# Optimization experiments

Measured on AMD Instinct MI355X. Metric: run time of the kernel, lower is better.

## Reference

```python
import jax, jax.numpy as jnp
import numpy as np

N_SEQ = 512      # n: number of generation steps (rows of x_tensor)
N_POOL = 4096    # candidate node pool size (rows of f_tensor / a_tensor)
N_FEAT = 20
E = 64           # n_node_embed
G = 128          # n_graph_embed
S = 16           # n_seq_embed
ALPHA = 20       # n_seq_alphabets


def setup_inputs() -> dict:
    key = jax.random.key(0)
    ks = jax.random.split(key, 16)
    f32 = jnp.float32

    def lin(k, fan_in, shape):
        return jax.random.normal(k, shape, f32) / jnp.sqrt(jnp.asarray(fan_in, f32))

    return {
        "x_tensor": jax.random.normal(ks[0], (N_SEQ, ALPHA), f32),
        "f_tensor": jax.random.normal(ks[1], (N_POOL, N_FEAT), f32),
        "a_tensor": jax.random.uniform(ks[2], (N_POOL, N_POOL), f32),
        "d_tensor": jax.random.uniform(ks[3], (N_POOL, N_POOL), f32),
        "w_feat": lin(ks[4], N_FEAT, (N_FEAT, E)),
        "b_feat": lin(ks[5], N_FEAT, (E,)),
        "w_gcn1": lin(ks[6], E, (E, E)),   # GCN W1, bias=False
        "w_gcn2": lin(ks[7], E, (E, E)),   # GCN W1, bias=False
        "w_graph": lin(ks[8], E, (E, G)),
        "b_graph": lin(ks[9], E, (G,)),
        "w_gate": lin(ks[10], E, (E, G)),
        "b_gate": lin(ks[11], E, (G,)),
        "w_edge": lin(ks[12], 2 * E + S + G, (2 * E + S + G, 1)),
        "b_edge": lin(ks[13], 2 * E + S + G, (1,)),
        "w_seq": lin(ks[14], ALPHA, (ALPHA, S)),
        "b_seq": lin(ks[15], ALPHA, (S,)),
    }


def reference(x_tensor, f_tensor, a_tensor, d_tensor,
              w_feat, b_feat, w_gcn1, w_gcn2,
              w_graph, b_graph, w_gate, b_gate,
              w_edge, b_edge, w_seq, b_seq):
    n = x_tensor.shape[0]
    Np = f_tensor.shape[0]
    e = w_feat.shape[1]
    g_dim = w_graph.shape[1]

    seq_embed = x_tensor @ w_seq + b_seq                 # [n, S]
    f_nodes_in = f_tensor @ w_feat + b_feat              # [Np, E]
    dAd = (d_tensor @ a_tensor) @ d_tensor               # gcn1: D A D
    h_nodes_in = (dAd @ jax.nn.relu(f_nodes_in)) @ w_gcn1  # [Np, E]

    # Chain graph at step k has k+1 nodes; A = I + sub/super diagonals.
    # Degrees: 1 (k==0), 2 at endpoints, 3 interior. Dh[k, i] = deg^{-1/2}, masked.
    ii = jnp.arange(n)
    kk = ii[:, None]
    jj = ii[None, :]
    deg = jnp.where((jj == 0) | (jj == kk), 2.0, 3.0)
    deg = jnp.where(kk == 0, 1.0, deg)
    Dh = jnp.where(jj <= kk, deg ** -0.5, 0.0).astype(x_tensor.dtype)  # [n, n]

    def step(carry, k):
        mask, idxs, h_last, h_graph = carry
        z = jnp.concatenate([
            h_nodes_in,
            jnp.broadcast_to(h_last, (Np, e)),
            jnp.broadcast_to(seq_embed[k], (Np, seq_embed.shape[1])),
            jnp.broadcast_to(h_graph, (Np, g_dim)),
        ], axis=1)                                        # [Np, 2E+S+G]
        score = ((jax.nn.relu(z) * mask[:, None]) @ w_edge)[:, 0] + b_edge[0]
        idx = jnp.argmax(score)
        mask = mask.at[idx].set(0.0)
        idxs = idxs.at[k].set(idx.astype(jnp.int32))

        # gcn2 on the chain graph over the k+1 selected nodes (band-structured).
        F_sel = f_nodes_in[idxs]                          # [n, E]; rows > k masked by dh
        dh = Dh[k]                                        # [n]
        gmat = dh[:, None] * F_sel
        g_up = jnp.pad(gmat, ((0, 1), (0, 0)))[1:]        # g[i+1]
        g_dn = jnp.pad(gmat, ((1, 0), (0, 0)))[:-1]       # g[i-1]
        dF = dh[:, None] * (gmat + g_up + g_dn)           # (D A D) F on the chain
        h_nodes = dF @ w_gcn2                             # [n, E]; rows > k are zero
        h_last_new = jnp.take(h_nodes, k, axis=0)

        valid = (jnp.arange(n) <= k).astype(h_nodes.dtype)[:, None]
        hg = h_nodes @ w_graph + b_graph
        gg = h_nodes @ w_gate + b_gate
        h_graph_new = jnp.sum(hg * jax.nn.sigmoid(gg) * valid, axis=0)
        return (mask, idxs, h_last_new, h_graph_new), score

    init = (jnp.ones(Np, x_tensor.dtype),
            jnp.zeros(n, jnp.int32),
            jnp.zeros(e, x_tensor.dtype),
            jnp.zeros(g_dim, x_tensor.dtype))
    (_, idxs, _, _), scores = jax.lax.scan(step, init, jnp.arange(n))
    return scores, idxs
```

## Files before the change

kernel.cpp:

```cpp
#include <hip/hip_runtime.h>
#include <math.h>

#define NPOOL 4096
#define NSEQ  512
#define NF    20
#define EDIM  64
#define GDIM  128
#define SDIM  16
#define ALPH  20
#define SPLITK 32
#define KSLICE (NPOOL / SPLITK)

__device__ __forceinline__ double relu_d(double x){ return x > 0.0 ? x : 0.0; }
__device__ __forceinline__ double sigm_d(double x){ return 1.0 / (1.0 + exp(-x)); }

__device__ __forceinline__ unsigned long long sortable_u64(double x) {
    x = x + 0.0;
    unsigned long long b = (unsigned long long)__double_as_longlong(x);
    return b ^ ((b >> 63) ? ~0ULL : 0x8000000000000000ULL);
}

__global__ __launch_bounds__(256) void k_prep(const float* __restrict__ f, const float* __restrict__ wf,
                       const float* __restrict__ bf, double* __restrict__ Fin, double* __restrict__ R,
                       double* __restrict__ T1z, double* __restrict__ T2z, double* __restrict__ T3z) {
    int t = blockIdx.x * 256 + threadIdx.x;
    int i = t >> 6, e = t & 63;
    double acc = (double)bf[e];
#pragma unroll
    for (int j = 0; j < NF; ++j)
        acc += (double)f[i * NF + j] * (double)wf[j * EDIM + e];
    Fin[t] = acc;
    R[t] = acc > 0.0 ? acc : 0.0;
    T1z[t] = 0.0; T2z[t] = 0.0; T3z[t] = 0.0;
}

__global__ __launch_bounds__(256) void k_seqe(const float* __restrict__ x, const float* __restrict__ wsq,
                       const float* __restrict__ bsq, double* __restrict__ seqe, int* __restrict__ rank) {
    int t = blockIdx.x * 256 + threadIdx.x;
    int k = t >> 4, s = t & 15;
    double acc = (double)bsq[s];
#pragma unroll
    for (int q = 0; q < ALPH; ++q)
        acc += (double)x[k * ALPH + q] * (double)wsq[q * SDIM + s];
    seqe[t] = acc;
    if (t < NPOOL) rank[t] = 1 << 30;
}

__global__ __launch_bounds__(256, 4) void gemm_f64_v5(const float* __restrict__ A, const double* __restrict__ B,
                                                      double* __restrict__ C) {
    __shared__ double As[32][66];
    __shared__ double Bs[32][66];
    int t  = threadIdx.x;
    int tx = t & 15;
    int ty = t >> 4;
    int row0 = blockIdx.x * 64;
    int k0   = blockIdx.y * KSLICE;
    double acc[4][4] = {};
    for (int kt = k0; kt < k0 + KSLICE; kt += 32) {
        {
            int r = t >> 2, kq = t & 3;
            const float* Ap = A + (size_t)(row0 + r) * NPOOL + kt + kq * 8;
            float4 f0 = *(const float4*)Ap;
            float4 f1 = *(const float4*)(Ap + 4);
            int kb = kq * 8;
            int rs = r ^ (kq << 2);
            As[kb + 0][rs] = (double)f0.x; As[kb + 1][rs] = (double)f0.y;
            As[kb + 2][rs] = (double)f0.z; As[kb + 3][rs] = (double)f0.w;
            As[kb + 4][rs] = (double)f1.x; As[kb + 5][rs] = (double)f1.y;
            As[kb + 6][rs] = (double)f1.z; As[kb + 7][rs] = (double)f1.w;
        }
#pragma unroll
        for (int it = 0; it < 8; ++it) {
            int l = t + 256 * it;
            int kr = l >> 6, cc = l & 63;
            Bs[kr][cc] = B[(size_t)(kt + kr) * 64 + cc];
        }
        __syncthreads();
#pragma unroll
        for (int kk = 0; kk < 32; ++kk) {
            int s = ((kk >> 3) & 3) << 2;
            double2 a01 = *(const double2*)&As[kk][(2 * ty +  0) ^ s];
            double2 a23 = *(const double2*)&As[kk][(2 * ty + 32) ^ s];
            double2 b01 = *(const double2*)&Bs[kk][2 * tx];
            double2 b23 = *(const double2*)&Bs[kk][2 * tx + 32];
            double a[4] = {a01.x, a01.y, a23.x, a23.y};
            double b[4] = {b01.x, b01.y, b23.x, b23.y};
#pragma unroll
            for (int i = 0; i < 4; ++i)
#pragma unroll
                for (int j = 0; j < 4; ++j)
                    acc[i][j] = fma(a[i], b[j], acc[i][j]);
        }
        __syncthreads();
    }
    int rr[4] = {2 * ty, 2 * ty + 1, 2 * ty + 32, 2 * ty + 33};
    int cc[4] = {2 * tx, 2 * tx + 1, 2 * tx + 32, 2 * tx + 33};
#pragma unroll
    for (int i = 0; i < 4; ++i)
#pragma unroll
        for (int j = 0; j < 4; ++j)
            unsafeAtomicAdd(&C[(size_t)(row0 + rr[i]) * 64 + cc[j]], acc[i][j]);
}

__global__ __launch_bounds__(256) void k_head(const double* __restrict__ T3, const float* __restrict__ w1,
                       const float* __restrict__ we, double* __restrict__ s) {
    __shared__ float w1s[64 * 64];
    int tt = threadIdx.x;
    for (int i = tt; i < 64 * 64; i += 256) w1s[i] = w1[i];
    __syncthreads();
    int row = (blockIdx.x * 256 + tt) >> 6;
    int e = tt & 63;
    const double* r = T3 + (size_t)row * 64;
    double h = 0.0;
#pragma unroll
    for (int c = 0; c < 64; ++c)
        h += r[c] * (double)w1s[c * 64 + e];
    double p = (h > 0.0 ? h : 0.0) * (double)we[e];
    for (int off = 32; off; off >>= 1) p += __shfl_down(p, off, 64);
    if (e == 0) s[row] = p;
}

__global__ __launch_bounds__(1024) void k_sort3(const double* __restrict__ s, int* __restrict__ order,
                        double* __restrict__ skey, int* __restrict__ orderB) {
    __shared__ unsigned long long P[NPOOL];
    __shared__ int idxF[NPOOL];
    __shared__ int fbS;
    int t = threadIdx.x;
    if (t == 0) fbS = 0;
    unsigned long long v[4];
#pragma unroll
    for (int i = 0; i < 4; ++i) {
        int e = 4 * t + i;
        unsigned long long srt = sortable_u64(s[e]);
        v[i] = ((~(srt >> 12)) << 12) | (unsigned long long)e;
    }

#define SHFL_ROUND(jj, kk)                                                        \
    {                                                                             \
        int lm = (int)((jj) >> 2);                                                \
        _Pragma("unroll")                                                         \
        for (int i = 0; i < 4; ++i) {                                             \
            unsigned long long p = (unsigned long long)__shfl_xor((long long)v[i], lm, 64); \
            unsigned e = 4u * (unsigned)t + (unsigned)i;                          \
            bool takeMin = (((e & (jj)) == 0u) == ((e & (kk)) == 0u));            \
            unsigned long long mn = v[i] < p ? v[i] : p;                          \
            unsigned long long mx = v[i] < p ? p : v[i];                          \
            v[i] = takeMin ? mn : mx;                                             \
        }                                                                         \
    }

#define LOCAL_ROUNDS(kk)                                                          \
    {                                                                             \
        if ((kk) >= 4) {                                                          \
            _Pragma("unroll")                                                     \
            for (int i = 0; i < 2; ++i) {                                         \
                unsigned e = 4u * (unsigned)t + (unsigned)i;                      \
                bool asc = ((e & (kk)) == 0u);                                    \
                unsigned long long a = v[i], b = v[i + 2];                        \
                bool sw = asc ? (a > b) : (a < b);                                \
                v[i] = sw ? b : a; v[i + 2] = sw ? a : b;                         \
            }                                                                     \
        }                                                                         \
        _Pragma("unroll")                                                         \
        for (int i = 0; i < 4; i += 2) {                                          \
            unsigned e = 4u * (unsigned)t + (unsigned)i;                          \
            bool asc = ((e & (kk)) == 0u);                                        \
            unsigned long long a = v[i], b = v[i + 1];                            \
            bool sw = asc ? (a > b) : (a < b);                                    \
            v[i] = sw ? b : a; v[i + 1] = sw ? a : b;                             \
        }                                                                         \
    }

    for (unsigned k = 2; k <= 256; k <<= 1) {
        for (unsigned j = k >> 1; j >= 4; j >>= 1) SHFL_ROUND(j, k)
        LOCAL_ROUNDS(k)
    }
    for (unsigned k = 512; k <= 4096; k <<= 1) {
        for (unsigned j = k >> 1; j >= 256; j >>= 1) {
            __syncthreads();
            P[4 * t + 0] = v[0]; P[4 * t + 1] = v[1];
            P[4 * t + 2] = v[2]; P[4 * t + 3] = v[3];
            __syncthreads();
            unsigned base = (4u * (unsigned)t) ^ j;
#pragma unroll
            for (int i = 0; i < 4; ++i) {
                unsigned e = 4u * (unsigned)t + (unsigned)i;
                unsigned long long p = P[base + i];
                bool takeMin = (((e & j) == 0u) == ((e & k) == 0u));
                unsigned long long mn = v[i] < p ? v[i] : p;
                unsigned long long mx = v[i] < p ? p : v[i];
                v[i] = takeMin ? mn : mx;
            }
        }
        for (unsigned j = 128; j >= 4; j >>= 1) SHFL_ROUND(j, k)
        LOCAL_ROUNDS(k)
    }
#undef SHFL_ROUND
#undef LOCAL_ROUNDS

    __syncthreads();
    P[4 * t + 0] = v[0]; P[4 * t + 1] = v[1];
    P[4 * t + 2] = v[2]; P[4 * t + 3] = v[3];
    __syncthreads();
    if (t < 512) {
        unsigned long long pa = P[t], pb = P[t + 1];
        if ((pa >> 12) == (pb >> 12)) {
            int ia = (int)(pa & 4095ULL), ib = (int)(pb & 4095ULL);
            if (sortable_u64(s[ia]) != sortable_u64(s[ib])) atomicOr(&fbS, 1);
        }
    }
    __syncthreads();
    if (fbS == 0) {
        if (t < NSEQ) {
            int id = (int)(P[t] & 4095ULL);
            order[t] = id; skey[t] = s[id]; orderB[t] = (int)(P[0] & 4095ULL);
        }
        return;
    }
    for (int i = t; i < NPOOL; i += 1024) { P[i] = sortable_u64(s[i]); idxF[i] = i; }
    __syncthreads();
    for (int k2 = 2; k2 <= NPOOL; k2 <<= 1) {
        for (int j = k2 >> 1; j > 0; j >>= 1) {
            for (int tt = t; tt < NPOOL; tt += 1024) {
                int l = tt ^ j;
                if (l > tt) {
                    unsigned long long ka = P[tt], kb = P[l];
                    int ia = idxF[tt], ib = idxF[l];
                    bool aBefore = (ka > kb) || (ka == kb && ia < ib);
                    bool asc = ((tt & k2) == 0);
                    if (asc ? !aBefore : aBefore) { P[tt] = kb; P[l] = ka; idxF[tt] = ib; idxF[l] = ia; }
                }
            }
            __syncthreads();
        }
    }
    for (int tt = t; tt < NSEQ; tt += 1024) {
        int id = idxF[tt];
        order[tt] = id; skey[tt] = s[id]; orderB[tt] = idxF[0];
    }
}

__global__ __launch_bounds__(256) void k_perk2(const double* __restrict__ Fin, const int* __restrict__ orderA,
                       const int* __restrict__ orderBv,
                       const float* __restrict__ w2, const float* __restrict__ wgr, const float* __restrict__ bgr,
                       const float* __restrict__ wga, const float* __restrict__ bga,
                       double* __restrict__ phi_inf, double* __restrict__ phi_pair, double* __restrict__ hlast) {
    const double r2 = 0.70710678118654752440;
    const double r3 = 0.57735026918962576451;
    __shared__ double u[4][64];
    __shared__ double comb[3][64];
    __shared__ double v[3][64];
    __shared__ double hgg[3][2][GDIM];
    int which = blockIdx.x >> 9;
    int k = blockIdx.x & (NSEQ - 1);
    const int* order = which ? orderBv : orderA;
    double* pi = phi_inf  + (size_t)which * NSEQ * GDIM;
    double* pp = phi_pair + (size_t)which * NSEQ * GDIM;
    double* hl = hlast    + (size_t)which * NSEQ * 64;
    int t = threadIdx.x;
    {
        int w = t >> 6, e = t & 63;
        int j = k - 3 + w;
        u[w][e] = (j >= 0) ? Fin[(size_t)order[j] * 64 + e] : 0.0;
    }
    __syncthreads();
    if (t < 192) {
        int w = t >> 6, e = t & 63;
        double dh_km3 = (k - 3 == 0) ? r2 : r3;
        double dh_km2 = (k - 2 == 0) ? r2 : r3;
        double dh_km1 = (k - 1 == 0) ? r2 : r3;
        double outer, c0, c1, c2, c3;
        if (w == 0) {
            outer = dh_km2; c0 = dh_km3; c1 = dh_km2; c2 = dh_km1; c3 = 0.0;
        } else if (w == 1) {
            outer = dh_km1; c0 = 0.0; c1 = dh_km2; c2 = dh_km1; c3 = r2;
        } else {
            if (k == 0) { outer = 1.0; c0 = c1 = c2 = 0.0; c3 = 1.0; }
            else        { outer = r2;  c0 = c1 = 0.0; c2 = dh_km1; c3 = r2; }
        }
        comb[w][e] = outer * (c0 * u[0][e] + c1 * u[1][e] + c2 * u[2][e] + c3 * u[3][e]);
    }
    __syncthreads();
    if (t < 192) {
        int w = t >> 6, e = t & 63;
        double acc = 0.0;
#pragma unroll
        for (int j = 0; j < 64; ++j)
            acc += comb[w][j] * (double)w2[j * 64 + e];
        v[w][e] = acc;
    }
    __syncthreads();
    for (int rep = 0; rep < 3; ++rep) {
        int d = t & 127, g = t >> 7;
        const float* W = g ? wga : wgr;
        const float* B = g ? bga : bgr;
        double acc = (double)B[d];
#pragma unroll
        for (int j = 0; j < 64; ++j)
            acc += v[rep][j] * (double)W[j * GDIM + d];
        hgg[rep][g][d] = acc;
    }
    __syncthreads();
    if (t < 128) {
        if (k >= 2) pi[(size_t)(k - 2) * GDIM + t] = hgg[0][0][t] * sigm_d(hgg[0][1][t]);
        double ppv = hgg[2][0][t] * sigm_d(hgg[2][1][t]);
        if (k >= 1) ppv += hgg[1][0][t] * sigm_d(hgg[1][1][t]);
        pp[(size_t)k * GDIM + t] = ppv;
    } else if (t < 192) {
        hl[(size_t)k * 64 + (t - 128)] = v[2][t - 128];
    }
}

__global__ __launch_bounds__(512) void k_scan2(const double* __restrict__ phi_inf, const double* __restrict__ phi_pair,
                       double* __restrict__ hgr) {
    __shared__ double sb[NSEQ];
    int which = blockIdx.x >> 7;
    int d = blockIdx.x & (GDIM - 1), t = threadIdx.x;
    const double* pi = phi_inf  + (size_t)which * NSEQ * GDIM;
    const double* pp = phi_pair + (size_t)which * NSEQ * GDIM;
    double* hg = hgr + (size_t)which * NSEQ * GDIM;
    sb[t] = (t >= 2) ? pi[(size_t)(t - 2) * GDIM + d] : 0.0;
    for (int off = 1; off < NSEQ; off <<= 1) {
        __syncthreads();
        double add = (t >= off) ? sb[t - off] : 0.0;
        __syncthreads();
        sb[t] += add;
    }
    __syncthreads();
    hg[(size_t)t * GDIM + d] = sb[t] + pp[(size_t)t * GDIM + d];
}

__global__ __launch_bounds__(64) void k_c2(const double* __restrict__ hlast, const double* __restrict__ hgr,
                   const double* __restrict__ seqe, const float* __restrict__ we,
                   double* __restrict__ cA, double* __restrict__ cB) {
    int which = blockIdx.x >> 9;
    int k = blockIdx.x & (NSEQ - 1), j = threadIdx.x;
    const double* hl = hlast + (size_t)which * NSEQ * 64;
    const double* hg = hgr   + (size_t)which * NSEQ * GDIM;
    double* c = which ? cB : cA;
    double ts = 0.0;
    if (k > 0) {
        ts += relu_d(hl[(size_t)(k - 1) * 64 + j]) * (double)we[64 + j];
        ts += relu_d(hg[(size_t)(k - 1) * GDIM + j]) * (double)we[144 + j];
        ts += relu_d(hg[(size_t)(k - 1) * GDIM + 64 + j]) * (double)we[208 + j];
    }
    if (j < 16) ts += relu_d(seqe[(size_t)k * SDIM + j]) * (double)we[128 + j];
    for (int off = 32; off; off >>= 1) ts += __shfl_down(ts, off, 64);
    if (j == 0) c[k] = ts;
}

__global__ __launch_bounds__(512) void k_verify2(const double* __restrict__ skey, const double* __restrict__ cA,
                         const double* __restrict__ cB, int* __restrict__ flagA, int* __restrict__ flagB) {
    __shared__ int bad;
    int t = threadIdx.x;
    if (t == 0) bad = 0;
    __syncthreads();
    if (blockIdx.x == 0) {
        if (t >= 1 && !(skey[t] + cA[t] > 0.0)) atomicOr(&bad, 1);
        __syncthreads();
        if (t == 0) flagA[0] = bad;
    } else {
        if (t >= 1 && (skey[1] + cB[t] > 0.0)) atomicOr(&bad, 1);
        __syncthreads();
        if (t == 0) flagB[0] = bad;
    }
}

__global__ __launch_bounds__(512) void k_select(const int* __restrict__ flagA, const int* __restrict__ flagB,
                        const double* __restrict__ cA, const double* __restrict__ cB,
                        const int* __restrict__ order, double* __restrict__ c,
                        int* __restrict__ idxs_sel, int* __restrict__ mode) {
    int t = threadIdx.x;
    if (flagA[0] == 0) {
        c[t] = cA[t]; idxs_sel[t] = order[t];
        if (t == 0) mode[0] = 0;
    } else if (flagB[0] == 0) {
        c[t] = cB[t]; idxs_sel[t] = order[0];
        if (t == 0) mode[0] = 1;
    } else {
        if (t == 0) mode[0] = 2;
    }
}

__global__ __launch_bounds__(256) void k_fallback(const int* __restrict__ mode,
        const double* __restrict__ Fin, const int* __restrict__ order, const double* __restrict__ skey,
        const double* __restrict__ seqe,
        const float* __restrict__ w2, const float* __restrict__ wgr, const float* __restrict__ bgr,
        const float* __restrict__ wga, const float* __restrict__ bga, const float* __restrict__ we,
        int* __restrict__ idxs_sel, double* __restrict__ c) {
    if (mode[0] != 2) return;
    const double r2 = 0.70710678118654752440;
    const double r3 = 0.57735026918962576451;
    __shared__ double u[4][64];
    __shared__ double comb[3][64];
    __shared__ double v[3][64];
    __shared__ double hgg[3][2][GDIM];
    __shared__ double Phi[GDIM], hgraph[GDIM], hlastS[64];
    __shared__ int selS, ptrS, minS_;
    int t = threadIdx.x;
    if (t < 64) { u[0][t] = u[1][t] = u[2][t] = u[3][t] = 0.0; hlastS[t] = 0.0; }
    if (t < 128) { Phi[t] = 0.0; hgraph[t] = 0.0; }
    if (t == 0) { ptrS = 0; minS_ = 0x7fffffff; }
    __syncthreads();
    for (int k = 0; k < NSEQ; ++k) {
        if (t < 64) {
            int j = t;
            double ts = relu_d(hlastS[j]) * (double)we[64 + j]
                      + relu_d(hgraph[j]) * (double)we[144 + j]
                      + relu_d(hgraph[64 + j]) * (double)we[208 + j];
            if (j < 16) ts += relu_d(seqe[(size_t)k * SDIM + j]) * (double)we[128 + j];
            for (int off = 32; off; off >>= 1) ts += __shfl_down(ts, off, 64);
            if (j == 0) {
                c[k] = ts;
                int ptr = ptrS, idx;
                if (ptr == 0) { idx = order[0]; minS_ = idx; ptrS = 1; }
                else if (skey[ptr] + ts > 0.0) {
                    idx = order[ptr];
                    if (idx < minS_) minS_ = idx;
                    ptrS = ptr + 1;
                } else idx = minS_;
                selS = idx;
                idxs_sel[k] = idx;
            }
        }
        __syncthreads();
        int idx = selS;
        if (t < 64) u[k & 3][t] = Fin[(size_t)idx * 64 + t];
        __syncthreads();
        if (t < 192) {
            int w = t >> 6, e = t & 63;
            double dh_km3 = (k - 3 == 0) ? r2 : r3;
            double dh_km2 = (k - 2 == 0) ? r2 : r3;
            double dh_km1 = (k - 1 == 0) ? r2 : r3;
            double outer, c0, c1, c2, c3;
            if (w == 0) {
                outer = dh_km2; c0 = dh_km3; c1 = dh_km2; c2 = dh_km1; c3 = 0.0;
            } else if (w == 1) {
                outer = dh_km1; c0 = 0.0; c1 = dh_km2; c2 = dh_km1; c3 = r2;
            } else {
                if (k == 0) { outer = 1.0; c0 = c1 = c2 = 0.0; c3 = 1.0; }
                else        { outer = r2;  c0 = c1 = 0.0; c2 = dh_km1; c3 = r2; }
            }
            double uu0 = u[(k - 3) & 3][e], uu1 = u[(k - 2) & 3][e], uu2 = u[(k - 1) & 3][e], uu3 = u[k & 3][e];
            comb[w][e] = outer * (c0 * uu0 + c1 * uu1 + c2 * uu2 + c3 * uu3);
        }
        __syncthreads();
        if (t < 192) {
            int w = t >> 6, e = t & 63;
            double acc = 0.0;
#pragma unroll
            for (int j = 0; j < 64; ++j)
                acc += comb[w][j] * (double)w2[j * 64 + e];
            v[w][e] = acc;
        }
        __syncthreads();
        for (int rep = 0; rep < 3; ++rep) {
            int d = t & 127, g = t >> 7;
            const float* W = g ? wga : wgr;
            const float* B = g ? bga : bgr;
            double acc = (double)B[d];
#pragma unroll
            for (int j = 0; j < 64; ++j)
                acc += v[rep][j] * (double)W[j * GDIM + d];
            hgg[rep][g][d] = acc;
        }
        __syncthreads();
        if (t < 128) {
            if (k >= 2) Phi[t] += hgg[0][0][t] * sigm_d(hgg[0][1][t]);
            double hg = Phi[t] + hgg[2][0][t] * sigm_d(hgg[2][1][t]);
            if (k >= 1) hg += hgg[1][0][t] * sigm_d(hgg[1][1][t]);
            hgraph[t] = hg;
        } else if (t < 192) {
            hlastS[t - 128] = v[2][t - 128];
        }
        __syncthreads();
    }
}

__global__ __launch_bounds__(256) void k_rank_set(const int* __restrict__ idxs_sel, int* __restrict__ rank,
                           float* __restrict__ out) {
    int t = blockIdx.x * 256 + threadIdx.x;
    if (t < NSEQ) {
        atomicMin(&rank[idxs_sel[t]], t);
        out[(size_t)NSEQ * NPOOL + t] = (float)idxs_sel[t];
    }
}

__global__ __launch_bounds__(256) void k_fill(const double* __restrict__ s, const double* __restrict__ c,
                       const int* __restrict__ rank, const float* __restrict__ be, float* __restrict__ out) {
    size_t t = (size_t)blockIdx.x * 256 + threadIdx.x;
    int k = (int)(t >> 12);
    int i = (int)(t & 4095);
    double bed = (double)be[0];
    bool masked = rank[i] < k;
    out[t] = masked ? (float)bed : (float)(s[i] + c[k] + bed);
}

extern "C" void kernel_launch(void* const* d_in, const int* in_sizes, int n_in,
                              void* d_out, int out_size, void* d_ws, size_t ws_size,
                              hipStream_t stream) {
    const float* x    = (const float*)d_in[0];
    const float* f    = (const float*)d_in[1];
    const float* amat = (const float*)d_in[2];
    const float* dmat = (const float*)d_in[3];
    const float* wf   = (const float*)d_in[4];
    const float* bf   = (const float*)d_in[5];
    const float* w1   = (const float*)d_in[6];
    const float* w2   = (const float*)d_in[7];
    const float* wgr  = (const float*)d_in[8];
    const float* bgr  = (const float*)d_in[9];
    const float* wga  = (const float*)d_in[10];
    const float* bga  = (const float*)d_in[11];
    const float* we   = (const float*)d_in[12];
    const float* be   = (const float*)d_in[13];
    const float* wsq  = (const float*)d_in[14];
    const float* bsq  = (const float*)d_in[15];
    float* out = (float*)d_out;

    char* p = (char*)d_ws;
    const size_t BIG = (size_t)NPOOL * 64 * sizeof(double);
    double* R    = (double*)p; p += BIG;
    double* Fin  = (double*)p; p += BIG;
    double* T1   = (double*)p; p += BIG;
    double* T2   = (double*)p; p += BIG;
    double* T3   = (double*)p; p += BIG;
    double* seqe = (double*)p; p += (size_t)NSEQ * SDIM * sizeof(double);
    double* s    = (double*)p; p += (size_t)NPOOL * sizeof(double);
    double* skey = (double*)p; p += (size_t)NSEQ * sizeof(double);
    double* phi_inf  = (double*)p; p += 2 * (size_t)NSEQ * GDIM * sizeof(double);
    double* phi_pair = (double*)p; p += 2 * (size_t)NSEQ * GDIM * sizeof(double);
    double* hgr   = (double*)p; p += 2 * (size_t)NSEQ * GDIM * sizeof(double);
    double* hlast = (double*)p; p += 2 * (size_t)NSEQ * 64 * sizeof(double);
    double* cA    = (double*)p; p += (size_t)NSEQ * sizeof(double);
    double* cB    = (double*)p; p += (size_t)NSEQ * sizeof(double);
    double* c     = (double*)p; p += (size_t)NSEQ * sizeof(double);
    int* order    = (int*)p; p += 2048;
    int* orderB   = (int*)p; p += 2048;
    int* idxs_sel = (int*)p; p += 2048;
    int* rank     = (int*)p; p += (size_t)NPOOL * sizeof(int);
    int* flagA    = (int*)p; p += 256;
    int* flagB    = (int*)p; p += 256;
    int* mode     = (int*)p; p += 256;

    dim3 ggrid(NPOOL / 64, SPLITK);

    k_prep<<<1024, 256, 0, stream>>>(f, wf, bf, Fin, R, T1, T2, T3);
    k_seqe<<<32, 256, 0, stream>>>(x, wsq, bsq, seqe, rank);

    gemm_f64_v5<<<ggrid, 256, 0, stream>>>(dmat, R, T1);
    gemm_f64_v5<<<ggrid, 256, 0, stream>>>(amat, T1, T2);
    gemm_f64_v5<<<ggrid, 256, 0, stream>>>(dmat, T2, T3);

    k_head<<<NPOOL / 4, 256, 0, stream>>>(T3, w1, we, s);
    k_sort3<<<1, 1024, 0, stream>>>(s, order, skey, orderB);

    k_perk2<<<2 * NSEQ, 256, 0, stream>>>(Fin, order, orderB, w2, wgr, bgr, wga, bga, phi_inf, phi_pair, hlast);
    k_scan2<<<2 * GDIM, 512, 0, stream>>>(phi_inf, phi_pair, hgr);
    k_c2<<<2 * NSEQ, 64, 0, stream>>>(hlast, hgr, seqe, we, cA, cB);
    k_verify2<<<2, 512, 0, stream>>>(skey, cA, cB, flagA, flagB);

    k_select<<<1, 512, 0, stream>>>(flagA, flagB, cA, cB, order, c, idxs_sel, mode);
    k_fallback<<<1, 256, 0, stream>>>(mode, Fin, order, skey, seqe, w2, wgr, bgr, wga, bga, we, idxs_sel, c);

    k_rank_set<<<2, 256, 0, stream>>>(idxs_sel, rank, out);
    k_fill<<<(NSEQ * NPOOL) / 256, 256, 0, stream>>>(s, c, rank, be, out);
}
```

Before: 560.8 us.

## Enlarge FP64 GEMM tile, keep A in LDS as float, prefetch next tile

Rewrites the split-K FP64 GEMM so each block computes a 128-row tile with 8x4 accumulators per thread and halves the split-K factor, which reduces B reloads and the number of atomic adds. The A tile is now stored in shared memory as float and converted to double when it is read, halving LDS footprint and store traffic. Global loads for the next K tile are issued into registers before the current tile's math runs, giving a register-staged double buffer. In exchange it uses more registers (launch bounds lowered to 2 blocks per CU), launches fewer blocks, and repeats the float-to-double conversion inside the inner loop.

```diff
diff --git a/kernel.cpp b/kernel.cpp
--- a/kernel.cpp
+++ b/kernel.cpp
@@ -8,7 +8,7 @@
 #define GDIM  128
 #define SDIM  16
 #define ALPH  20
-#define SPLITK 32
+#define SPLITK 16
 #define KSLICE (NPOOL / SPLITK)
 
 __device__ __forceinline__ double relu_d(double x){ return x > 0.0 ? x : 0.0; }
@@ -46,60 +46,92 @@
     if (t < NPOOL) rank[t] = 1 << 30;
 }
 
-__global__ __launch_bounds__(256, 4) void gemm_f64_v5(const float* __restrict__ A, const double* __restrict__ B,
+__global__ __launch_bounds__(256, 2) void gemm_f64_v7(const float* __restrict__ A, const double* __restrict__ B,
                                                       double* __restrict__ C) {
-    __shared__ double As[32][66];
+    __shared__ float  As[32][132];
     __shared__ double Bs[32][66];
     int t  = threadIdx.x;
     int tx = t & 15;
     int ty = t >> 4;
-    int row0 = blockIdx.x * 64;
+    int row0 = blockIdx.x * 128;
     int k0   = blockIdx.y * KSLICE;
-    double acc[4][4] = {};
+    int kq = t & 3, kb = kq << 3;
+    int ar = t >> 2;
+
+    double acc[8][4] = {};
+    float4  pa[2][2];
+    double2 pb[4];
+
+#define LOADG(KT)                                                                  \
+    {                                                                              \
+        _Pragma("unroll")                                                          \
+        for (int h = 0; h < 2; ++h) {                                              \
+            const float* Ap = A + (size_t)(row0 + ar + 64 * h) * NPOOL + (KT) + kq * 8; \
+            pa[h][0] = *(const float4*)Ap;                                         \
+            pa[h][1] = *(const float4*)(Ap + 4);                                   \
+        }                                                                          \
+        _Pragma("unroll")                                                          \
+        for (int it = 0; it < 4; ++it) {                                           \
+            int e = 2 * t + 512 * it;                                              \
+            pb[it] = *(const double2*)&B[(size_t)((KT) + (e >> 6)) * 64 + (e & 63)]; \
+        }                                                                          \
+    }
+
+#define STORELDS()                                                                 \
+    {                                                                              \
+        _Pragma("unroll")                                                          \
+        for (int h = 0; h < 2; ++h) {                                              \
+            int rs = (ar + 64 * h) ^ (kq << 2);                                    \
+            As[kb + 0][rs] = pa[h][0].x; As[kb + 1][rs] = pa[h][0].y;              \
+            As[kb + 2][rs] = pa[h][0].z; As[kb + 3][rs] = pa[h][0].w;              \
+            As[kb + 4][rs] = pa[h][1].x; As[kb + 5][rs] = pa[h][1].y;              \
+            As[kb + 6][rs] = pa[h][1].z; As[kb + 7][rs] = pa[h][1].w;              \
+        }                                                                          \
+        _Pragma("unroll")                                                          \
+        for (int it = 0; it < 4; ++it) {                                           \
+            int e = 2 * t + 512 * it;                                              \
+            *(double2*)&Bs[e >> 6][e & 63] = pb[it];                               \
+        }                                                                          \
+    }
+
+    LOADG(k0)
+    STORELDS()
+    __syncthreads();
+
     for (int kt = k0; kt < k0 + KSLICE; kt += 32) {
-        {
-            int r = t >> 2, kq = t & 3;
-            const float* Ap = A + (size_t)(row0 + r) * NPOOL + kt + kq * 8;
-            float4 f0 = *(const float4*)Ap;
-            float4 f1 = *(const float4*)(Ap + 4);
-            int kb = kq * 8;
-            int rs = r ^ (kq << 2);
-            As[kb + 0][rs] = (double)f0.x; As[kb + 1][rs] = (double)f0.y;
-            As[kb + 2][rs] = (double)f0.z; As[kb + 3][rs] = (double)f0.w;
-            As[kb + 4][rs] = (double)f1.x; As[kb + 5][rs] = (double)f1.y;
-            As[kb + 6][rs] = (double)f1.z; As[kb + 7][rs] = (double)f1.w;
-        }
-#pragma unroll
-        for (int it = 0; it < 8; ++it) {
-            int l = t + 256 * it;
-            int kr = l >> 6, cc = l & 63;
-            Bs[kr][cc] = B[(size_t)(kt + kr) * 64 + cc];
-        }
-        __syncthreads();
+        bool more = (kt + 32 < k0 + KSLICE);
+        if (more) LOADG(kt + 32)
 #pragma unroll
         for (int kk = 0; kk < 32; ++kk) {
-            int s = ((kk >> 3) & 3) << 2;
-            double2 a01 = *(const double2*)&As[kk][(2 * ty +  0) ^ s];
-            double2 a23 = *(const double2*)&As[kk][(2 * ty + 32) ^ s];
+            const int kqr = kk >> 3;
+            int abase = 8 * (ty ^ (kqr >> 1));
+            float4 alo = *(const float4*)&As[kk][abase];
+            float4 ahi = *(const float4*)&As[kk][abase + 4];
+            if (kqr & 1) { float4 tmp = alo; alo = ahi; ahi = tmp; }
+            double a[8] = {(double)alo.x, (double)alo.y, (double)alo.z, (double)alo.w,
+                           (double)ahi.x, (double)ahi.y, (double)ahi.z, (double)ahi.w};
             double2 b01 = *(const double2*)&Bs[kk][2 * tx];
             double2 b23 = *(const double2*)&Bs[kk][2 * tx + 32];
-            double a[4] = {a01.x, a01.y, a23.x, a23.y};
             double b[4] = {b01.x, b01.y, b23.x, b23.y};
 #pragma unroll
-            for (int i = 0; i < 4; ++i)
+            for (int i = 0; i < 8; ++i)
 #pragma unroll
                 for (int j = 0; j < 4; ++j)
                     acc[i][j] = fma(a[i], b[j], acc[i][j]);
         }
         __syncthreads();
-    }
-    int rr[4] = {2 * ty, 2 * ty + 1, 2 * ty + 32, 2 * ty + 33};
+        if (more) STORELDS()
+        __syncthreads();
+    }
+#undef LOADG
+#undef STORELDS
+
     int cc[4] = {2 * tx, 2 * tx + 1, 2 * tx + 32, 2 * tx + 33};
 #pragma unroll
-    for (int i = 0; i < 4; ++i)
+    for (int i = 0; i < 8; ++i)
 #pragma unroll
         for (int j = 0; j < 4; ++j)
-            unsafeAtomicAdd(&C[(size_t)(row0 + rr[i]) * 64 + cc[j]], acc[i][j]);
+            unsafeAtomicAdd(&C[(size_t)(row0 + 8 * ty + i) * 64 + cc[j]], acc[i][j]);
 }
 
 __global__ __launch_bounds__(256) void k_head(const double* __restrict__ T3, const float* __restrict__ w1,
@@ -542,14 +574,14 @@
     int* flagB    = (int*)p; p += 256;
     int* mode     = (int*)p; p += 256;
 
-    dim3 ggrid(NPOOL / 64, SPLITK);
+    dim3 ggrid(NPOOL / 128, SPLITK);
 
     k_prep<<<1024, 256, 0, stream>>>(f, wf, bf, Fin, R, T1, T2, T3);
     k_seqe<<<32, 256, 0, stream>>>(x, wsq, bsq, seqe, rank);
 
-    gemm_f64_v5<<<ggrid, 256, 0, stream>>>(dmat, R, T1);
-    gemm_f64_v5<<<ggrid, 256, 0, stream>>>(amat, T1, T2);
-    gemm_f64_v5<<<ggrid, 256, 0, stream>>>(dmat, T2, T3);
+    gemm_f64_v7<<<ggrid, 256, 0, stream>>>(dmat, R, T1);
+    gemm_f64_v7<<<ggrid, 256, 0, stream>>>(amat, T1, T2);
+    gemm_f64_v7<<<ggrid, 256, 0, stream>>>(dmat, T2, T3);
 
     k_head<<<NPOOL / 4, 256, 0, stream>>>(T3, w1, we, s);
     k_sort3<<<1, 1024, 0, stream>>>(s, order, skey, orderB);
```

After: 2.118 ms. +277.6%, slower.

## Enlarge FP64 GEMM tile to 128 rows, store A as float in LDS

Applied to the files above, without the earlier changes.

The split-K FP64 GEMM now gives each block 128 rows instead of 64, and each thread accumulates 8x4 outputs instead of 4x4. This halves the number of B-tile loads per output and raises the FMA-to-LDS-load ratio. The A tile stays float in shared memory and is converted to double at use, which keeps LDS size about the same; B loads are widened to double2. The cost is more accumulator registers under launch_bounds(256,4), half as many blocks, and a new swizzle scheme that must stay bank-conflict free.

```diff
diff --git a/kernel.cpp b/kernel.cpp
--- a/kernel.cpp
+++ b/kernel.cpp
@@ -46,60 +46,65 @@
     if (t < NPOOL) rank[t] = 1 << 30;
 }
 
-__global__ __launch_bounds__(256, 4) void gemm_f64_v5(const float* __restrict__ A, const double* __restrict__ B,
+__global__ __launch_bounds__(256, 4) void gemm_f64_v8(const float* __restrict__ A, const double* __restrict__ B,
                                                       double* __restrict__ C) {
-    __shared__ double As[32][66];
+    __shared__ float  As[32][132];
     __shared__ double Bs[32][66];
     int t  = threadIdx.x;
     int tx = t & 15;
     int ty = t >> 4;
-    int row0 = blockIdx.x * 64;
+    int row0 = blockIdx.x * 128;
     int k0   = blockIdx.y * KSLICE;
-    double acc[4][4] = {};
+    int kq = t & 3, kb = kq << 3;
+    int ar = t >> 2;
+
+    double acc[8][4] = {};
+
     for (int kt = k0; kt < k0 + KSLICE; kt += 32) {
-        {
-            int r = t >> 2, kq = t & 3;
-            const float* Ap = A + (size_t)(row0 + r) * NPOOL + kt + kq * 8;
+#pragma unroll
+        for (int h = 0; h < 2; ++h) {
+            const float* Ap = A + (size_t)(row0 + ar + 64 * h) * NPOOL + kt + kq * 8;
             float4 f0 = *(const float4*)Ap;
             float4 f1 = *(const float4*)(Ap + 4);
-            int kb = kq * 8;
-            int rs = r ^ (kq << 2);
-            As[kb + 0][rs] = (double)f0.x; As[kb + 1][rs] = (double)f0.y;
-            As[kb + 2][rs] = (double)f0.z; As[kb + 3][rs] = (double)f0.w;
-            As[kb + 4][rs] = (double)f1.x; As[kb + 5][rs] = (double)f1.y;
-            As[kb + 6][rs] = (double)f1.z; As[kb + 7][rs] = (double)f1.w;
-        }
-#pragma unroll
-        for (int it = 0; it < 8; ++it) {
-            int l = t + 256 * it;
-            int kr = l >> 6, cc = l & 63;
-            Bs[kr][cc] = B[(size_t)(kt + kr) * 64 + cc];
+            int rs = (ar + 64 * h) ^ (kq << 2);
+            As[kb + 0][rs] = f0.x; As[kb + 1][rs] = f0.y;
+            As[kb + 2][rs] = f0.z; As[kb + 3][rs] = f0.w;
+            As[kb + 4][rs] = f1.x; As[kb + 5][rs] = f1.y;
+            As[kb + 6][rs] = f1.z; As[kb + 7][rs] = f1.w;
+        }
+#pragma unroll
+        for (int it = 0; it < 4; ++it) {
+            int e = 2 * t + 512 * it;
+            *(double2*)&Bs[e >> 6][e & 63] = *(const double2*)&B[(size_t)(kt + (e >> 6)) * 64 + (e & 63)];
         }
         __syncthreads();
 #pragma unroll
         for (int kk = 0; kk < 32; ++kk) {
-            int s = ((kk >> 3) & 3) << 2;
-            double2 a01 = *(const double2*)&As[kk][(2 * ty +  0) ^ s];
-            double2 a23 = *(const double2*)&As[kk][(2 * ty + 32) ^ s];
+            const int kqr = kk >> 3;
+            int abase = 8 * (ty ^ (kqr >> 1));
+            float4 alo = *(const float4*)&As[kk][abase];
+            float4 ahi = *(const float4*)&As[kk][abase + 4];
+            if (kqr & 1) { float4 tmp = alo; alo = ahi; ahi = tmp; }
+            double a[8] = {(double)alo.x, (double)alo.y, (double)alo.z, (double)alo.w,
+                           (double)ahi.x, (double)ahi.y, (double)ahi.z, (double)ahi.w};
             double2 b01 = *(const double2*)&Bs[kk][2 * tx];
             double2 b23 = *(const double2*)&Bs[kk][2 * tx + 32];
-            double a[4] = {a01.x, a01.y, a23.x, a23.y};
             double b[4] = {b01.x, b01.y, b23.x, b23.y};
 #pragma unroll
-            for (int i = 0; i < 4; ++i)
+            for (int i = 0; i < 8; ++i)
 #pragma unroll
                 for (int j = 0; j < 4; ++j)
                     acc[i][j] = fma(a[i], b[j], acc[i][j]);
         }
         __syncthreads();
     }
-    int rr[4] = {2 * ty, 2 * ty + 1, 2 * ty + 32, 2 * ty + 33};
+
     int cc[4] = {2 * tx, 2 * tx + 1, 2 * tx + 32, 2 * tx + 33};
 #pragma unroll
-    for (int i = 0; i < 4; ++i)
+    for (int i = 0; i < 8; ++i)
 #pragma unroll
         for (int j = 0; j < 4; ++j)
-            unsafeAtomicAdd(&C[(size_t)(row0 + rr[i]) * 64 + cc[j]], acc[i][j]);
+            unsafeAtomicAdd(&C[(size_t)(row0 + 8 * ty + i) * 64 + cc[j]], acc[i][j]);
 }
 
 __global__ __launch_bounds__(256) void k_head(const double* __restrict__ T3, const float* __restrict__ w1,
@@ -542,14 +547,14 @@
     int* flagB    = (int*)p; p += 256;
     int* mode     = (int*)p; p += 256;
 
-    dim3 ggrid(NPOOL / 64, SPLITK);
+    dim3 ggrid(NPOOL / 128, SPLITK);
 
     k_prep<<<1024, 256, 0, stream>>>(f, wf, bf, Fin, R, T1, T2, T3);
     k_seqe<<<32, 256, 0, stream>>>(x, wsq, bsq, seqe, rank);
 
-    gemm_f64_v5<<<ggrid, 256, 0, stream>>>(dmat, R, T1);
-    gemm_f64_v5<<<ggrid, 256, 0, stream>>>(amat, T1, T2);
-    gemm_f64_v5<<<ggrid, 256, 0, stream>>>(dmat, T2, T3);
+    gemm_f64_v8<<<ggrid, 256, 0, stream>>>(dmat, R, T1);
+    gemm_f64_v8<<<ggrid, 256, 0, stream>>>(amat, T1, T2);
+    gemm_f64_v8<<<ggrid, 256, 0, stream>>>(dmat, T2, T3);
 
     k_head<<<NPOOL / 4, 256, 0, stream>>>(T3, w1, we, s);
     k_sort3<<<1, 1024, 0, stream>>>(s, order, skey, orderB);
```

Result: slower. 619.9 us (+10.5%).
